# Optimization experiments

Hardware: AMD Instinct MI355X
Metric: run time of the kernel (lower is better)

Reference implementation:

```python
import jax, jax.numpy as jnp
import numpy as np

P, M, N, D, H, DFF = 20000, 20000, 16, 128, 8, 512
DPH = D // H
EPS = 1e-6
LN_EPS = 1e-5


def vn_linear(x, w):
    # x: (..., C_in, 3), w: (C_in, C_out) -> (..., C_out, 3)
    return jnp.einsum('...ci,co->...oi', x, w)


def vn_layernorm(x, gamma, beta):
    # x: (P, D, 3); layernorm over channel dim on vector norms, rescale directions
    n = jnp.linalg.norm(x, axis=-1)                      # (P, D)
    mu = jnp.mean(n, axis=-1, keepdims=True)
    var = jnp.var(n, axis=-1, keepdims=True)
    n_hat = (n - mu) / jnp.sqrt(var + LN_EPS) * gamma + beta
    return x * (n_hat / (n + EPS))[..., None]


def vn_relu(q, k):
    # VN nonlinearity: q, k: (..., C, 3); project q off negative half-space of k
    dot = jnp.sum(q * k, axis=-1, keepdims=True)         # (..., C, 1)
    ksq = jnp.sum(k * k, axis=-1, keepdims=True)
    return jnp.where(dot >= 0, q, q - (dot / (ksq + EPS)) * k)


def setup_inputs():
    key = jax.random.key(0)
    ks = jax.random.split(key, 24)
    s = lambda i, shp, scale: (jax.random.normal(ks[i], shp, jnp.float32) * scale)
    inp = {
        'tgt': s(0, (P, D * 3), 1.0),
        'memory': s(1, (M, D * 3), 1.0),
        'sh': s(2, (P, N + 1, 3), 1.0),
        'dist_atten': s(3, (P, N, H), 1.0),
        'Wq': s(4, (D, D), D ** -0.5),
        'Wk': s(5, (D, D), D ** -0.5),
        'Wv': s(6, (D, D), D ** -0.5),
        'Wo': s(7, (D, D), D ** -0.5),
        'g_w1': s(8, (D, H), D ** -0.5),
        'g_b1': jnp.zeros((H,), jnp.float32),
        'g_w2': s(9, (H, H), H ** -0.5),
        'g_b2': jnp.zeros((H,), jnp.float32),
        'ln1_g': jnp.ones((D,), jnp.float32),
        'ln1_b': jnp.zeros((D,), jnp.float32),
        'ln2_g': jnp.ones((D,), jnp.float32),
        'ln2_b': jnp.zeros((D,), jnp.float32),
        'ff_w1': s(10, (D, DFF), D ** -0.5),
        'ff_d1': s(11, (D, DFF), D ** -0.5),
        'ff_w2': s(12, (DFF, D), DFF ** -0.5),
        'index_pair': jax.random.randint(ks[13], (P, N), 0, M),
        'cnt1': jax.random.randint(ks[14], (P,), 0, N),
        'cnt2': jax.random.randint(ks[15], (P,), 0, N),
    }
    return inp


def reference(tgt, memory, sh, dist_atten, Wq, Wk, Wv, Wo,
              g_w1, g_b1, g_w2, g_b2, ln1_g, ln1_b, ln2_g, ln2_b,
              ff_w1, ff_d1, ff_w2, index_pair, cnt1, cnt2):
    x = tgt.reshape(P, D, 3)
    mem = memory.reshape(M, D, 3)
    q = vn_linear(x, Wq)                                  # (P, D, 3)
    k_all = vn_linear(mem, Wk)                            # (M, D, 3)
    v_all = vn_linear(mem, Wv)
    # irregular neighbor gather (ca_attention_mapper_v3)
    k = k_all[index_pair]                                 # (P, N, D, 3)
    v = v_all[index_pair]                                 # (P, N, D, 3)
    sh_n = sh[:, 1:].reshape(P, N, 1, 3)                  # drop l=0 term
    # multi-head dot attention on 3D vector features
    dot_atten = jnp.einsum('phdi,pnhdi->pnh',
                           q.reshape(P, H, DPH, 3),
                           k.reshape(P, N, H, DPH, 3))
    # spherical-harmonic position bias
    pos = jnp.sum((k - q[:, None]) * sh_n, axis=-1)       # (P, N, D)
    pos = jax.nn.relu(pos @ g_w1 + g_b1) @ g_w2 + g_b2    # (P, N, H)
    atten = (dot_atten + pos + dist_atten) / (DPH ** 0.5)
    atten = jax.nn.softmax(atten, axis=1)                 # softmax over neighbors
    tgt2 = jnp.einsum('pnh,pnhci->phci', atten,
                      v.reshape(P, N, H, DPH, 3)).reshape(P, D, 3)
    tgt2 = vn_linear(tgt2, Wo)
    y = vn_layernorm(x + tgt2, ln1_g, ln1_b)
    h1 = vn_relu(vn_linear(y, ff_w1), vn_linear(y, ff_d1))
    ff_out = vn_linear(h1, ff_w2)
    y = vn_layernorm(y + ff_out, ln2_g, ln2_b)
    return y.reshape(P, D * 3)
```

## Files before the change

### kernel.cpp

```cpp
#include <hip/hip_runtime.h>

#define PP 20000

typedef short short8 __attribute__((ext_vector_type(8)));
typedef float floatx4 __attribute__((ext_vector_type(4)));

__device__ __forceinline__ unsigned int bf16_rne_bits(float x){
    unsigned int xb = __float_as_uint(x);
    return (xb + 0x7FFFu + ((xb >> 16) & 1u)) & 0xFFFF0000u;
}
__device__ __forceinline__ void split2(float x, short &h, short &l){
    unsigned int hb = bf16_rne_bits(x);
    h = (short)(hb >> 16);
    float r = x - __uint_as_float(hb);
    l = (short)(bf16_rne_bits(r) >> 16);
}

__device__ __align__(16) short g_ff1[32*8192];
__device__ __align__(16) short g_ff2[16*8192];
__device__ __align__(16) short g_qkvo[4][4*8192];

__global__ __launch_bounds__(256) void prep_weights(
    const float* __restrict__ Wq, const float* __restrict__ Wk,
    const float* __restrict__ Wv, const float* __restrict__ Wo,
    const float* __restrict__ W1, const float* __restrict__ Wd,
    const float* __restrict__ W2)
{
    const int tid = blockIdx.x*256 + threadIdx.x;
    for (int e = tid; e < 65536; e += 16384){
        int j = e & 7, kg = (e>>3) & 15, n = (e>>7) & 15, ch = e >> 11;
        int k = kg*8 + j, col = ch*16 + n;
        int pos = n*128 + ((kg ^ (n&7)) << 3) + j;
        short h, l;
        split2(W1[(size_t)k*512 + col], h, l);
        g_ff1[ch*8192 + pos]        = h;
        g_ff1[ch*8192 + 2048 + pos] = l;
        split2(Wd[(size_t)k*512 + col], h, l);
        g_ff1[ch*8192 + 4096 + pos] = h;
        g_ff1[ch*8192 + 6144 + pos] = l;
    }
    for (int e = tid; e < 65536; e += 16384){
        int w = e & 31, n2 = (e>>5) & 127, pair = e >> 12;
        int lslot = (w>>3) ^ ((n2>>1)&3);
        int k = pair*32 + lslot*8 + (w&7);
        short h, l; split2(W2[(size_t)k*128 + n2], h, l);
        g_ff2[pair*8192 + n2*32 + w]        = h;
        g_ff2[pair*8192 + 4096 + n2*32 + w] = l;
    }
    for (int e = tid; e < 65536; e += 16384){
        int w = e & 127, col = (e>>7) & 31, ch = (e>>12) & 3, wg = e >> 14;
        int lslot = (w>>3) ^ (col&7);
        int k = lslot*8 + (w&7);
        const float* Wsrc = (wg==0)?Wq:(wg==1)?Wk:(wg==2)?Wv:Wo;
        short h, l; split2(Wsrc[(size_t)k*128 + ch*32 + col], h, l);
        g_qkvo[wg][ch*8192 + col*128 + w]        = h;
        g_qkvo[wg][ch*8192 + 4096 + col*128 + w] = l;
    }
}

__global__ __launch_bounds__(256) void vn_gemm_mfma(const float* __restrict__ in,
    int widx, float* __restrict__ out)
{
    __shared__ __align__(16) char pool[32768];
    short* Ysh = (short*)pool;
    short* Ysl = (short*)(pool + 16384);
    short* Bh  = (short*)pool;
    short* Bl  = (short*)(pool + 8192);

    const int tid  = threadIdx.x;
    const int wv   = tid >> 6;
    const int lane = tid & 63;
    const int mrow = lane & 15;
    const int kgrp = lane >> 4;
    const int p0   = blockIdx.x * 16;

    for (int f = tid; f < 2048; f += 256){
        int row = (f >> 7)*4 + 3, k = f & 127;
        Ysh[row*128 + k] = 0; Ysl[row*128 + k] = 0;
    }
    #pragma unroll
    for (int t = 0; t < 6; ++t){
        int f = tid + t*256;
        float4 w4 = *(const float4*)(in + (size_t)p0*384 + f*4);
        int e = f*4, pl = e/384, rem = e - pl*384;
        float vv4[4] = {w4.x, w4.y, w4.z, w4.w};
        #pragma unroll
        for (int j=0;j<4;++j){
            int c = (rem+j)/3, i = (rem+j) - c*3;
            int row = pl*4 + i;
            int idx = row*128 + (((c>>3) ^ (row&7)) << 3) + (c&7);
            short h, l; split2(vv4[j], h, l);
            Ysh[idx] = h; Ysl[idx] = l;
        }
    }
    __syncthreads();
    short8 ahf[4], alf[4];
    {
        const int arow = wv*16 + mrow;
        #pragma unroll
        for (int ks=0;ks<4;++ks){
            int slot = ks*4 + kgrp;
            int aoff = arow*128 + ((slot ^ (arow&7)) << 3);
            ahf[ks] = *(const short8*)(Ysh + aoff);
            alf[ks] = *(const short8*)(Ysl + aoff);
        }
    }

    const short* gW = g_qkvo[widx];
    for (int ch = 0; ch < 4; ++ch){
        __syncthreads();
        #pragma unroll
        for (int t=0;t<4;++t)
            ((short8*)pool)[tid + t*256] =
                ((const short8*)(gW + ch*8192))[tid + t*256];
        __syncthreads();

        #pragma unroll
        for (int ntl=0; ntl<2; ++ntl){
            floatx4 acc = {0.f,0.f,0.f,0.f};
            const int lcol = ntl*16 + mrow;
            #pragma unroll
            for (int ks=0;ks<4;++ks){
                int slot = ks*4 + kgrp;
                int boff = lcol*128 + ((slot ^ (mrow&7)) << 3);
                short8 bh = *(const short8*)(Bh + boff);
                short8 bl = *(const short8*)(Bl + boff);
                acc = __builtin_amdgcn_mfma_f32_16x16x32_bf16(ahf[ks], bh, acc, 0,0,0);
                acc = __builtin_amdgcn_mfma_f32_16x16x32_bf16(ahf[ks], bl, acc, 0,0,0);
                acc = __builtin_amdgcn_mfma_f32_16x16x32_bf16(alf[ks], bh, acc, 0,0,0);
            }
            const int p = p0 + wv*4 + kgrp;
            const int o = ch*32 + ntl*16 + mrow;
            size_t base = (size_t)p*384 + (size_t)o*3;
            out[base    ] = acc[0];
            out[base + 1] = acc[1];
            out[base + 2] = acc[2];
        }
    }
}

__global__ __launch_bounds__(256) void vn_gemm_ln_mfma(const float* __restrict__ in,
    const float* __restrict__ resid, const float* __restrict__ gamma,
    const float* __restrict__ beta, float* __restrict__ out)
{
    __shared__ __align__(16) char pool[32768];
    short* Ysh = (short*)pool;
    short* Ysl = (short*)(pool + 16384);
    short* Bh  = (short*)pool;
    short* Bl  = (short*)(pool + 8192);

    const int tid  = threadIdx.x;
    const int wv   = tid >> 6;
    const int lane = tid & 63;
    const int mrow = lane & 15;
    const int kgrp = lane >> 4;
    const int p0   = blockIdx.x * 16;

    for (int f = tid; f < 2048; f += 256){
        int row = (f >> 7)*4 + 3, k = f & 127;
        Ysh[row*128 + k] = 0; Ysl[row*128 + k] = 0;
    }
    #pragma unroll
    for (int t = 0; t < 6; ++t){
        int f = tid + t*256;
        float4 w4 = *(const float4*)(in + (size_t)p0*384 + f*4);
        int e = f*4, pl = e/384, rem = e - pl*384;
        float vv4[4] = {w4.x, w4.y, w4.z, w4.w};
        #pragma unroll
        for (int j=0;j<4;++j){
            int c = (rem+j)/3, i = (rem+j) - c*3;
            int row = pl*4 + i;
            int idx = row*128 + (((c>>3) ^ (row&7)) << 3) + (c&7);
            short h, l; split2(vv4[j], h, l);
            Ysh[idx] = h; Ysl[idx] = l;
        }
    }
    __syncthreads();
    short8 ahf[4], alf[4];
    {
        const int arow = wv*16 + mrow;
        #pragma unroll
        for (int ks=0;ks<4;++ks){
            int slot = ks*4 + kgrp;
            int aoff = arow*128 + ((slot ^ (arow&7)) << 3);
            ahf[ks] = *(const short8*)(Ysh + aoff);
            alf[ks] = *(const short8*)(Ysl + aoff);
        }
    }

    const int p = p0 + wv*4 + kgrp;
    float rx[8], ry[8], rz[8];
    const short* gW = g_qkvo[3];
    #pragma unroll
    for (int ch = 0; ch < 4; ++ch){
        __syncthreads();
        #pragma unroll
        for (int t=0;t<4;++t)
            ((short8*)pool)[tid + t*256] =
                ((const short8*)(gW + ch*8192))[tid + t*256];
        __syncthreads();

        #pragma unroll
        for (int ntl=0; ntl<2; ++ntl){
            floatx4 acc = {0.f,0.f,0.f,0.f};
            const int lcol = ntl*16 + mrow;
            #pragma unroll
            for (int ks=0;ks<4;++ks){
                int slot = ks*4 + kgrp;
                int boff = lcol*128 + ((slot ^ (mrow&7)) << 3);
                short8 bh = *(const short8*)(Bh + boff);
                short8 bl = *(const short8*)(Bl + boff);
                acc = __builtin_amdgcn_mfma_f32_16x16x32_bf16(ahf[ks], bh, acc, 0,0,0);
                acc = __builtin_amdgcn_mfma_f32_16x16x32_bf16(ahf[ks], bl, acc, 0,0,0);
                acc = __builtin_amdgcn_mfma_f32_16x16x32_bf16(alf[ks], bh, acc, 0,0,0);
            }
            const int s = ch*2 + ntl;
            const int o = ch*32 + ntl*16 + mrow;
            size_t base = (size_t)p*384 + (size_t)o*3;
            rx[s] = resid[base]   + acc[0];
            ry[s] = resid[base+1] + acc[1];
            rz[s] = resid[base+2] + acc[2];
        }
    }

    float nrm[8], s1 = 0.f, s2 = 0.f;
    #pragma unroll
    for (int s=0;s<8;++s){
        float n = sqrtf(rx[s]*rx[s] + ry[s]*ry[s] + rz[s]*rz[s]);
        nrm[s] = n; s1 += n; s2 += n*n;
    }
    #pragma unroll
    for (int m=1; m<16; m<<=1){
        s1 += __shfl_xor(s1, m);
        s2 += __shfl_xor(s2, m);
    }
    float mu  = s1*(1.f/128.f);
    float var = s2*(1.f/128.f) - mu*mu;
    float inv = rsqrtf(var + 1e-5f);
    #pragma unroll
    for (int s=0;s<8;++s){
        int o = (s>>1)*32 + (s&1)*16 + mrow;
        size_t base = (size_t)p*384 + (size_t)o*3;
        float nh = (nrm[s] - mu)*inv*gamma[o] + beta[o];
        float sc = nh/(nrm[s] + 1e-6f);
        out[base] = rx[s]*sc; out[base+1] = ry[s]*sc; out[base+2] = rz[s]*sc;
    }
}

__global__ __launch_bounds__(128) void attn_score(
    const float* qf, const float* __restrict__ kf,
    const float* __restrict__ sh, const float* __restrict__ dist, const int* __restrict__ idxp,
    const float* __restrict__ gw1, const float* __restrict__ gb1,
    const float* __restrict__ gw2, const float* __restrict__ gb2,
    float* att)
{
    const int p = blockIdx.x, c = threadIdx.x;
    __shared__ __align__(16) float dot_s[16*132];
    __shared__ __align__(16) float pos_s[16*132];
    __shared__ float sh_s[48];
    __shared__ int   nidx[16];
    __shared__ __align__(16) float w1t[8*132];
    __shared__ float w2_s[64], b1_s[8], b2_s[8];
    __shared__ float u2_s[16*8], logit_s[16*8];

    if (c < 16) nidx[c] = idxp[p*16 + c];
    if (c < 48) sh_s[c] = sh[(size_t)p*51 + 3 + c];
    #pragma unroll
    for (int f = c; f < 1024; f += 128){
        int th2 = f >> 7, cc2 = f & 127;
        w1t[th2*132 + cc2] = gw1[cc2*8 + th2];
    }
    if (c < 64) w2_s[c] = gw2[c];
    if (c < 8){ b1_s[c]=gb1[c]; b2_s[c]=gb2[c]; }
    size_t qa = (size_t)p*384 + c*3;
    float qx = qf[qa], qy = qf[qa+1], qz = qf[qa+2];
    __syncthreads();

    for (int n=0;n<16;++n){
        size_t kbase = (size_t)nidx[n]*384 + c*3;
        float kx = kf[kbase], ky = kf[kbase+1], kz = kf[kbase+2];
        dot_s[n*132 + c] = kx*qx + ky*qy + kz*qz;
        pos_s[n*132 + c] = (kx-qx)*sh_s[n*3] + (ky-qy)*sh_s[n*3+1] + (kz-qz)*sh_s[n*3+2];
    }
    __syncthreads();

    const int tn = c >> 3, th = c & 7;
    const float* drow = dot_s + tn*132 + th*16;
    float4 d0 = *(const float4*)(drow);
    float4 d1 = *(const float4*)(drow + 4);
    float4 d2 = *(const float4*)(drow + 8);
    float4 d3 = *(const float4*)(drow + 12);
    float dsum = (d0.x+d0.y+d0.z+d0.w) + (d1.x+d1.y+d1.z+d1.w)
               + (d2.x+d2.y+d2.z+d2.w) + (d3.x+d3.y+d3.z+d3.w);

    float uj = b1_s[th];
    const float* prow = pos_s + tn*132;
    const float* wrow = w1t  + th*132;
    #pragma unroll 8
    for (int cc=0; cc<128; cc+=4){
        float4 pv = *(const float4*)(prow + cc);
        float4 wv = *(const float4*)(wrow + cc);
        uj = fmaf(pv.x, wv.x, uj);
        uj = fmaf(pv.y, wv.y, uj);
        uj = fmaf(pv.z, wv.z, uj);
        uj = fmaf(pv.w, wv.w, uj);
    }
    u2_s[tn*8+th] = fmaxf(uj, 0.f);
    __syncthreads();

    float l = b2_s[th];
    #pragma unroll
    for (int j=0;j<8;++j) l += u2_s[tn*8+j]*w2_s[j*8+th];
    l += dsum + dist[(size_t)p*128 + tn*8 + th];
    logit_s[tn*8+th] = l * 0.25f;
    __syncthreads();

    if (c < 8){
        float mx = -3.0e38f;
        #pragma unroll
        for (int n=0;n<16;++n) mx = fmaxf(mx, logit_s[n*8+c]);
        float e[16], ssum = 0.f;
        #pragma unroll
        for (int n=0;n<16;++n){ e[n] = __expf(logit_s[n*8+c]-mx); ssum += e[n]; }
        float inv = 1.f/ssum;
        #pragma unroll
        for (int n=0;n<16;++n) att[(size_t)p*384 + n*8 + c] = e[n]*inv;
    }
}

__global__ __launch_bounds__(128) void attn_apply(const float* __restrict__ vv,
                                                  const int* __restrict__ idxp,
                                                  float* io)
{
    const int p = blockIdx.x, c = threadIdx.x;
    __shared__ float att_s[128];
    __shared__ int   nidx[16];
    if (c < 16) nidx[c] = idxp[p*16 + c];
    att_s[c] = io[(size_t)p*384 + c];
    __syncthreads();

    const int h = c >> 4;
    float ax=0.f, ay=0.f, az=0.f;
    #pragma unroll
    for (int n=0;n<16;++n){
        float wgt = att_s[n*8+h];
        size_t vb = (size_t)nidx[n]*384 + c*3;
        ax += wgt*vv[vb]; ay += wgt*vv[vb+1]; az += wgt*vv[vb+2];
    }
    size_t ob = (size_t)p*384 + c*3;
    io[ob] = ax; io[ob+1] = ay; io[ob+2] = az;
}

__global__ __launch_bounds__(256,2) void vn_ff_mfma(const float* __restrict__ in,
    const float* __restrict__ l2g, const float* __restrict__ l2b,
    float* __restrict__ out)
{
    __shared__ __align__(16) char pool[40960];
    short* Ws1h = (short*)(pool);
    short* Ws1l = (short*)(pool + 4096);
    short* Wsdh = (short*)(pool + 8192);
    short* Wsdl = (short*)(pool + 12288);
    short* Ws2h = (short*)(pool + 16384);
    short* Ws2l = (short*)(pool + 24576);
    short* Hsh  = (short*)(pool + 32768);
    short* Hsl  = (short*)(pool + 36864);
    short* Ysh  = (short*)(pool);
    short* Ysl  = (short*)(pool + 16384);

    const int tid  = threadIdx.x;
    const int wv   = tid >> 6;
    const int lane = tid & 63;
    const int mrow = lane & 15;
    const int kgrp = lane >> 4;
    const int p0   = blockIdx.x * 16;

    for (int f = tid; f < 2048; f += 256){
        int row = (f >> 7)*4 + 3, k = f & 127;
        Ysh[row*128 + k] = 0; Ysl[row*128 + k] = 0;
    }
    #pragma unroll
    for (int t = 0; t < 6; ++t){
        int f = tid + t*256;
        float4 w4 = *(const float4*)(in + (size_t)p0*384 + f*4);
        int e = f*4, pl = e/384, rem = e - pl*384;
        float vv4[4] = {w4.x, w4.y, w4.z, w4.w};
        #pragma unroll
        for (int j=0;j<4;++j){
            int c = (rem+j)/3, i = (rem+j) - c*3;
            int row = pl*4 + i;
            int idx = row*128 + (((c>>3) ^ (row&7)) << 3) + (c&7);
            short h, l; split2(vv4[j], h, l);
            Ysh[idx] = h; Ysl[idx] = l;
        }
    }
    __syncthreads();
    short8 ahf[4], alf[4];
    {
        const int arow = wv*16 + mrow;
        #pragma unroll
        for (int ks=0;ks<4;++ks){
            int slot = ks*4 + kgrp;
            int aoff = arow*128 + ((slot ^ (arow&7)) << 3);
            ahf[ks] = *(const short8*)(Ysh + aoff);
            alf[ks] = *(const short8*)(Ysl + aoff);
        }
    }

    floatx4 acc2[8];
    #pragma unroll
    for (int nt=0;nt<8;++nt) acc2[nt] = (floatx4){0.f,0.f,0.f,0.f};

    for (int ch = 0; ch < 32; ++ch){
        __syncthreads();
        #pragma unroll
        for (int t=0;t<4;++t)
            ((short8*)pool)[tid + t*256] =
                ((const short8*)(g_ff1 + ch*8192))[tid + t*256];
        if ((ch & 1) == 0){
            #pragma unroll
            for (int t=0;t<4;++t)
                ((short8*)(pool + 16384))[tid + t*256] =
                    ((const short8*)(g_ff2 + (ch>>1)*8192))[tid + t*256];
        }
        __syncthreads();

        floatx4 aU = {0.f,0.f,0.f,0.f}, aD = {0.f,0.f,0.f,0.f};
        #pragma unroll
        for (int ks=0;ks<4;++ks){
            int slot = ks*4 + kgrp;
            int boff = mrow*128 + ((slot ^ (mrow&7)) << 3);
            short8 b1h = *(const short8*)(Ws1h + boff);
            short8 b1l = *(const short8*)(Ws1l + boff);
            short8 bdh = *(const short8*)(Wsdh + boff);
            short8 bdl = *(const short8*)(Wsdl + boff);
            aU = __builtin_amdgcn_mfma_f32_16x16x32_bf16(ahf[ks], b1h, aU, 0,0,0);
            aU = __builtin_amdgcn_mfma_f32_16x16x32_bf16(ahf[ks], b1l, aU, 0,0,0);
            aU = __builtin_amdgcn_mfma_f32_16x16x32_bf16(alf[ks], b1h, aU, 0,0,0);
            aD = __builtin_amdgcn_mfma_f32_16x16x32_bf16(ahf[ks], bdh, aD, 0,0,0);
            aD = __builtin_amdgcn_mfma_f32_16x16x32_bf16(ahf[ks], bdl, aD, 0,0,0);
            aD = __builtin_amdgcn_mfma_f32_16x16x32_bf16(alf[ks], bdh, aD, 0,0,0);
        }

        {
            float ux=aU[0], uy=aU[1], uz=aU[2];
            float dx=aD[0], dy=aD[1], dz=aD[2];
            float dot = ux*dx + uy*dy + uz*dz;
            float ksq = dx*dx + dy*dy + dz*dz;
            if (dot < 0.f){
                float fc = dot/(ksq + 1e-6f);
                ux -= fc*dx; uy -= fc*dy; uz -= fc*dz;
            }
            int col  = (ch & 1)*16 + mrow;
            int slot = col >> 3, cl = col & 7;
            float hv[4] = {ux, uy, uz, 0.f};
            #pragma unroll
            for (int r=0;r<4;++r){
                int row = wv*16 + kgrp*4 + r;
                int idx = row*32 + ((slot ^ ((row>>1)&3)) << 3) + cl;
                short h, l; split2(hv[r], h, l);
                Hsh[idx] = h; Hsl[idx] = l;
            }
        }

        if (ch & 1){
            const int arow2 = wv*16 + mrow;
            int aoff = arow2*32 + ((kgrp ^ ((arow2>>1)&3)) << 3);
            short8 ah = *(const short8*)(Hsh + aoff);
            short8 al = *(const short8*)(Hsl + aoff);
            #pragma unroll
            for (int nt=0;nt<8;++nt){
                int bcol = nt*16 + mrow;
                int boff = bcol*32 + ((kgrp ^ ((bcol>>1)&3)) << 3);
                short8 bh = *(const short8*)(Ws2h + boff);
                short8 bl = *(const short8*)(Ws2l + boff);
                acc2[nt] = __builtin_amdgcn_mfma_f32_16x16x32_bf16(ah, bh, acc2[nt], 0,0,0);
                acc2[nt] = __builtin_amdgcn_mfma_f32_16x16x32_bf16(ah, bl, acc2[nt], 0,0,0);
                acc2[nt] = __builtin_amdgcn_mfma_f32_16x16x32_bf16(al, bh, acc2[nt], 0,0,0);
            }
        }
    }

    const int p = p0 + wv*4 + kgrp;
    float nrm[8];
    float s1 = 0.f, s2 = 0.f;
    #pragma unroll
    for (int nt=0;nt<8;++nt){
        int o = nt*16 + mrow;
        size_t base = (size_t)p*384 + (size_t)o*3;
        float rx = in[base]   + acc2[nt][0];
        float ry = in[base+1] + acc2[nt][1];
        float rz = in[base+2] + acc2[nt][2];
        float n = sqrtf(rx*rx + ry*ry + rz*rz);
        nrm[nt] = n;
        s1 += n; s2 += n*n;
    }
    #pragma unroll
    for (int m=1; m<16; m<<=1){
        s1 += __shfl_xor(s1, m);
        s2 += __shfl_xor(s2, m);
    }
    float mu  = s1*(1.f/128.f);
    float var = s2*(1.f/128.f) - mu*mu;
    float inv = rsqrtf(var + 1e-5f);
    #pragma unroll
    for (int nt=0;nt<8;++nt){
        int o = nt*16 + mrow;
        size_t base = (size_t)p*384 + (size_t)o*3;
        float rx = in[base]   + acc2[nt][0];
        float ry = in[base+1] + acc2[nt][1];
        float rz = in[base+2] + acc2[nt][2];
        float nh = (nrm[nt] - mu)*inv*l2g[o] + l2b[o];
        float sc = nh/(nrm[nt] + 1e-6f);
        out[base] = rx*sc; out[base+1] = ry*sc; out[base+2] = rz*sc;
    }
}

extern "C" void kernel_launch(void* const* d_in, const int* in_sizes, int n_in,
                              void* d_out, int out_size, void* d_ws, size_t ws_size,
                              hipStream_t stream)
{
    const float* tgt  = (const float*)d_in[0];
    const float* mem  = (const float*)d_in[1];
    const float* sh   = (const float*)d_in[2];
    const float* dist = (const float*)d_in[3];
    const float* Wq   = (const float*)d_in[4];
    const float* Wk   = (const float*)d_in[5];
    const float* Wv   = (const float*)d_in[6];
    const float* Wo   = (const float*)d_in[7];
    const float* gw1  = (const float*)d_in[8];
    const float* gb1  = (const float*)d_in[9];
    const float* gw2  = (const float*)d_in[10];
    const float* gb2  = (const float*)d_in[11];
    const float* ln1g = (const float*)d_in[12];
    const float* ln1b = (const float*)d_in[13];
    const float* ln2g = (const float*)d_in[14];
    const float* ln2b = (const float*)d_in[15];
    const float* fw1  = (const float*)d_in[16];
    const float* fd1  = (const float*)d_in[17];
    const float* fw2  = (const float*)d_in[18];
    const int*   idx  = (const int*)d_in[19];

    float* wsf = (float*)d_ws;
    float* outf = (float*)d_out;

    prep_weights<<<64,256,0,stream>>>(Wq, Wk, Wv, Wo, fw1, fd1, fw2);

    vn_gemm_mfma<<<1250,256,0,stream>>>(mem, 1, wsf);
    vn_gemm_mfma<<<1250,256,0,stream>>>(tgt, 0, outf);
    attn_score<<<PP,128,0,stream>>>(outf, wsf, sh, dist, idx, gw1, gb1, gw2, gb2, outf);
    vn_gemm_mfma<<<1250,256,0,stream>>>(mem, 2, wsf);
    attn_apply<<<PP,128,0,stream>>>(wsf, idx, outf);
    vn_gemm_ln_mfma<<<1250,256,0,stream>>>(outf, tgt, ln1g, ln1b, wsf);
    vn_ff_mfma<<<1250,256,0,stream>>>(wsf, ln2g, ln2b, outf);
}
```

Baseline: 493.7 us.

## Fuse attention score and apply kernels; store V padded to float4

Merges attn_score and attn_apply into one per-point kernel, so the softmax weights stay in shared memory instead of going out to global memory and being read back, and one launch is removed. The V projection is computed before the fused kernel and written to a new global buffer padded to 4 floats per vector, so the neighbor gather becomes one aligned float4 load. Padding V raises its write and read volume by a third, and adds a static device buffer of about 41 MB.

New measurement: 505.7 us. 2.4% more time.

```diff
diff --git a/kernel.cpp b/kernel.cpp
--- a/kernel.cpp
+++ b/kernel.cpp
@@ -19,6 +19,7 @@
 __device__ __align__(16) short g_ff1[32*8192];
 __device__ __align__(16) short g_ff2[16*8192];
 __device__ __align__(16) short g_qkvo[4][4*8192];
+__device__ __align__(16) float g_vvf[PP*128*4];
 
 __global__ __launch_bounds__(256) void prep_weights(
     const float* __restrict__ Wq, const float* __restrict__ Wk,
@@ -58,7 +59,8 @@
     }
 }
 
-__global__ __launch_bounds__(256) void vn_gemm_mfma(const float* __restrict__ in,
+template<int VOUT>
+__global__ __launch_bounds__(256) void vn_gemm_mfma_t(const float* __restrict__ in,
     int widx, float* __restrict__ out)
 {
     __shared__ __align__(16) char pool[32768];
@@ -131,10 +133,16 @@
             }
             const int p = p0 + wv*4 + kgrp;
             const int o = ch*32 + ntl*16 + mrow;
-            size_t base = (size_t)p*384 + (size_t)o*3;
-            out[base    ] = acc[0];
-            out[base + 1] = acc[1];
-            out[base + 2] = acc[2];
+            if (VOUT == 0){
+                size_t base = (size_t)p*384 + (size_t)o*3;
+                out[base    ] = acc[0];
+                out[base + 1] = acc[1];
+                out[base + 2] = acc[2];
+            } else {
+                float4 v4;
+                v4.x = acc[0]; v4.y = acc[1]; v4.z = acc[2]; v4.w = 0.f;
+                *(float4*)(g_vvf + ((size_t)p*128 + o)*4) = v4;
+            }
         }
     }
 }
@@ -247,12 +255,11 @@
     }
 }
 
-__global__ __launch_bounds__(128) void attn_score(
-    const float* qf, const float* __restrict__ kf,
+__global__ __launch_bounds__(128) void attn_fused(
+    float* io, const float* __restrict__ kf,
     const float* __restrict__ sh, const float* __restrict__ dist, const int* __restrict__ idxp,
     const float* __restrict__ gw1, const float* __restrict__ gb1,
-    const float* __restrict__ gw2, const float* __restrict__ gb2,
-    float* att)
+    const float* __restrict__ gw2, const float* __restrict__ gb2)
 {
     const int p = blockIdx.x, c = threadIdx.x;
     __shared__ __align__(16) float dot_s[16*132];
@@ -262,6 +269,7 @@
     __shared__ __align__(16) float w1t[8*132];
     __shared__ float w2_s[64], b1_s[8], b2_s[8];
     __shared__ float u2_s[16*8], logit_s[16*8];
+    __shared__ float att_s[128];
 
     if (c < 16) nidx[c] = idxp[p*16 + c];
     if (c < 48) sh_s[c] = sh[(size_t)p*51 + 3 + c];
@@ -273,7 +281,7 @@
     if (c < 64) w2_s[c] = gw2[c];
     if (c < 8){ b1_s[c]=gb1[c]; b2_s[c]=gb2[c]; }
     size_t qa = (size_t)p*384 + c*3;
-    float qx = qf[qa], qy = qf[qa+1], qz = qf[qa+2];
+    float qx = io[qa], qy = io[qa+1], qz = io[qa+2];
     __syncthreads();
 
     for (int n=0;n<16;++n){
@@ -324,19 +332,8 @@
         for (int n=0;n<16;++n){ e[n] = __expf(logit_s[n*8+c]-mx); ssum += e[n]; }
         float inv = 1.f/ssum;
         #pragma unroll
-        for (int n=0;n<16;++n) att[(size_t)p*384 + n*8 + c] = e[n]*inv;
-    }
-}
-
-__global__ __launch_bounds__(128) void attn_apply(const float* __restrict__ vv,
-                                                  const int* __restrict__ idxp,
-                                                  float* io)
-{
-    const int p = blockIdx.x, c = threadIdx.x;
-    __shared__ float att_s[128];
-    __shared__ int   nidx[16];
-    if (c < 16) nidx[c] = idxp[p*16 + c];
-    att_s[c] = io[(size_t)p*384 + c];
+        for (int n=0;n<16;++n) att_s[n*8+c] = e[n]*inv;
+    }
     __syncthreads();
 
     const int h = c >> 4;
@@ -344,8 +341,10 @@
     #pragma unroll
     for (int n=0;n<16;++n){
         float wgt = att_s[n*8+h];
-        size_t vb = (size_t)nidx[n]*384 + c*3;
-        ax += wgt*vv[vb]; ay += wgt*vv[vb+1]; az += wgt*vv[vb+2];
+        float4 v4 = *(const float4*)(g_vvf + ((size_t)nidx[n]*128 + c)*4);
+        ax += wgt*v4.x;
+        ay += wgt*v4.y;
+        az += wgt*v4.z;
     }
     size_t ob = (size_t)p*384 + c*3;
     io[ob] = ax; io[ob+1] = ay; io[ob+2] = az;
@@ -545,11 +544,10 @@
 
     prep_weights<<<64,256,0,stream>>>(Wq, Wk, Wv, Wo, fw1, fd1, fw2);
 
-    vn_gemm_mfma<<<1250,256,0,stream>>>(mem, 1, wsf);
-    vn_gemm_mfma<<<1250,256,0,stream>>>(tgt, 0, outf);
-    attn_score<<<PP,128,0,stream>>>(outf, wsf, sh, dist, idx, gw1, gb1, gw2, gb2, outf);
-    vn_gemm_mfma<<<1250,256,0,stream>>>(mem, 2, wsf);
-    attn_apply<<<PP,128,0,stream>>>(wsf, idx, outf);
+    vn_gemm_mfma_t<0><<<1250,256,0,stream>>>(mem, 1, wsf);
+    vn_gemm_mfma_t<1><<<1250,256,0,stream>>>(mem, 2, nullptr);
+    vn_gemm_mfma_t<0><<<1250,256,0,stream>>>(tgt, 0, outf);
+    attn_fused<<<PP,128,0,stream>>>(outf, wsf, sh, dist, idx, gw1, gb1, gw2, gb2);
     vn_gemm_ln_mfma<<<1250,256,0,stream>>>(outf, tgt, ln1g, ln1b, wsf);
     vn_ff_mfma<<<1250,256,0,stream>>>(wsf, ln2g, ln2b, outf);
 }
```
